# Performance work log

Hardware: AMD Instinct MI355X
Metric: run time of the kernel (lower is better)

Reference implementation:

```python
import jax, jax.numpy as jnp
import numpy as np

N_NODES = 50000
N_EDGES = 600000
IN_DIM = 128
HID = 128
OUT_DIM = 40
NUM_REL = 3
LN_EPS = 1e-5


def layer_norm(x, g, b):
    mu = jnp.mean(x, axis=-1, keepdims=True)
    var = jnp.var(x, axis=-1, keepdims=True)
    return (x - mu) * jax.lax.rsqrt(var + LN_EPS) * g + b


def rgcn_conv(x, edge_index, edge_type, w_rel, w_root, bias, aggr):
    """PyG-style RGCNConv: out = x @ W_root + bias + sum_r aggr_r(x_src @ W_r)."""
    src, dst = edge_index[0], edge_index[1]
    out = x @ w_root + bias                      # [N, F_out]
    for r in range(NUM_REL):                     # small fixed relation loop
        h = x @ w_rel[r]                         # transform-then-gather: [N, F_out]
        msg = h[src]                             # [E, F_out]
        mask = (edge_type == r)[:, None]
        if aggr == 'add':
            msg = jnp.where(mask, msg, 0.0)
            agg = jax.ops.segment_sum(msg, dst, num_segments=N_NODES)
        else:  # 'max'; empty segments -> 0 (matches PyG scatter_reduce include_self=False over zeros)
            msg = jnp.where(mask, msg, -jnp.inf)
            agg = jax.ops.segment_max(msg, dst, num_segments=N_NODES)
            agg = jnp.where(jnp.isfinite(agg), agg, 0.0)
        out = out + agg
    return out


def setup_inputs() -> dict:
    key = jax.random.key(0)
    ks = jax.random.split(key, 16)
    f32 = jnp.float32
    def lin(k, fan_in, shape):
        return jax.random.normal(k, shape, dtype=f32) / np.sqrt(fan_in)
    inp = {
        'x': jax.random.normal(ks[0], (N_NODES, IN_DIM), dtype=f32),
        'edge_index': jax.random.randint(ks[1], (2, N_EDGES), 0, N_NODES),
        'edge_type': jax.random.randint(ks[2], (N_EDGES,), 0, NUM_REL),
        # conv1
        'w1_rel': lin(ks[3], IN_DIM, (NUM_REL, IN_DIM, HID)),
        'w1_root': lin(ks[4], IN_DIM, (IN_DIM, HID)),
        'b1': jnp.zeros((HID,), f32),
        'ln1_g': jnp.ones((HID,), f32), 'ln1_b': jnp.zeros((HID,), f32),
        # conv2
        'w2_rel': lin(ks[5], HID, (NUM_REL, HID, HID)),
        'w2_root': lin(ks[6], HID, (HID, HID)),
        'b2': jnp.zeros((HID,), f32),
        'ln2_g': jnp.ones((HID,), f32), 'ln2_b': jnp.zeros((HID,), f32),
        # classifier
        'cw1': lin(ks[7], HID, (HID, HID)), 'cb1': jnp.zeros((HID,), f32),
        'cln1_g': jnp.ones((HID,), f32), 'cln1_b': jnp.zeros((HID,), f32),
        'cw2': lin(ks[8], HID, (HID, HID // 2)), 'cb2': jnp.zeros((HID // 2,), f32),
        'cln2_g': jnp.ones((HID // 2,), f32), 'cln2_b': jnp.zeros((HID // 2,), f32),
        'cw3': lin(ks[9], HID // 2, (HID // 2, OUT_DIM)), 'cb3': jnp.zeros((OUT_DIM,), f32),
    }
    return inp


def reference(x, edge_index, edge_type,
              w1_rel, w1_root, b1, ln1_g, ln1_b,
              w2_rel, w2_root, b2, ln2_g, ln2_b,
              cw1, cb1, cln1_g, cln1_b,
              cw2, cb2, cln2_g, cln2_b,
              cw3, cb3):
    # eval mode: edge dropout and feature dropout are identity
    h = rgcn_conv(x, edge_index, edge_type, w1_rel, w1_root, b1, 'add')
    h = jax.nn.relu(layer_norm(h, ln1_g, ln1_b))
    x1 = h
    h = rgcn_conv(x1, edge_index, edge_type, w2_rel, w2_root, b2, 'max')
    h = jax.nn.relu(layer_norm(h, ln2_g, ln2_b))
    h = h + x1 * 0.2
    # classifier MLP
    h = jax.nn.gelu(layer_norm(h @ cw1 + cb1, cln1_g, cln1_b), approximate=False)
    h = jax.nn.gelu(layer_norm(h @ cw2 + cb2, cln2_g, cln2_b), approximate=False)
    h = h @ cw3 + cb3
    return jax.nn.log_softmax(h, axis=1)
```

## Files before the change

kernel.cpp:

```cpp
#include <hip/hip_runtime.h>
#include <hip/hip_bf16.h>
#include <math.h>


typedef __attribute__((ext_vector_type(8))) short bf16x8;
typedef __attribute__((ext_vector_type(4))) float f32x4;
typedef unsigned short ushort_t;

__device__ __forceinline__ ushort_t bf16rne(float v) {
    unsigned u = __float_as_uint(v);
    return (ushort_t)((u + 0x7FFFu + ((u >> 16) & 1u)) >> 16);
}

__device__ __forceinline__ void split_bf16(float v, ushort_t& h, ushort_t& l) {
    ushort_t hu = bf16rne(v);
    float hf = __uint_as_float((unsigned)hu << 16);
    h = hu;
    l = bf16rne(v - hf);
}

__device__ __forceinline__ float bf2f(unsigned u16) {
    return __uint_as_float(u16 << 16);
}

__device__ __forceinline__ float4 unpack_bf4(uint2 u) {
    return make_float4(bf2f(u.x & 0xFFFFu), bf2f(u.x >> 16),
                       bf2f(u.y & 0xFFFFu), bf2f(u.y >> 16));
}

__device__ __forceinline__ uint2 pack_bf4(float4 v) {
    uint2 o;
    o.x = (unsigned)bf16rne(v.x) | ((unsigned)bf16rne(v.y) << 16);
    o.y = (unsigned)bf16rne(v.z) | ((unsigned)bf16rne(v.w) << 16);
    return o;
}

__device__ __forceinline__ void conv_body128(const float* __restrict__ W,
                                             ushort_t* __restrict__ out,
                                             int idx) {
    constexpr int NCF = 8;
    constexpr size_t PST = (size_t)4 * NCF * 512;
    int l = idx & 63;
    int cf = (idx >> 6) & 7;
    int ks = idx >> 9;
    int col = cf * 16 + (l & 15);
    int k0 = ks * 32 + (l >> 4) * 8;
    size_t base = (((size_t)ks * NCF + cf) * 64 + l) * 8;
#pragma unroll
    for (int j = 0; j < 8; ++j) {
        ushort_t h, lo_;
        split_bf16(W[(size_t)(k0 + j) * 128 + col], h, lo_);
        out[base + j] = h;
        out[PST + base + j] = lo_;
    }
}

__global__ __launch_bounds__(256) void convert_all(
    const float* __restrict__ w1_root, const float* __restrict__ w1_rel,
    const float* __restrict__ w2_root, const float* __restrict__ w2_rel,
    const float* __restrict__ cw1, const float* __restrict__ cw2,
    ushort_t* __restrict__ wfb) {
    int b = blockIdx.x;
    if (b < 72) {
        const float* src;
        int slot;
        if (b < 8)       { slot = 0;              src = w1_root; }
        else if (b < 32) { int r = (b - 8) >> 3;  slot = 1 + r; src = w1_rel + (size_t)r * 16384; }
        else if (b < 40) { slot = 4;              src = w2_root; }
        else if (b < 64) { int r = (b - 40) >> 3; slot = 5 + r; src = w2_rel + (size_t)r * 16384; }
        else             { slot = 8;              src = cw1; }
        int lb = (b < 8) ? b : (b < 32) ? ((b - 8) & 7) : (b < 40) ? (b - 32)
               : (b < 64) ? ((b - 40) & 7) : (b - 64);
        conv_body128(src, wfb + (size_t)slot * 32768, lb * 256 + threadIdx.x);
    } else {
        constexpr int NCF = 4;
        constexpr size_t PST = (size_t)4 * NCF * 512;
        int idx = (b - 72) * 256 + threadIdx.x;
        ushort_t* out = wfb + (size_t)9 * 32768;
        int l = idx & 63;
        int cf = (idx >> 6) & 3;
        int ks = idx >> 8;
        int col = cf * 16 + (l & 15);
        int k0 = ks * 32 + (l >> 4) * 8;
        size_t base = (((size_t)ks * NCF + cf) * 64 + l) * 8;
#pragma unroll
        for (int j = 0; j < 8; ++j) {
            ushort_t h, lo_;
            split_bf16(cw2[(size_t)(k0 + j) * 64 + col], h, lo_);
            out[base + j] = h;
            out[PST + base + j] = lo_;
        }
    }
}

__global__ __launch_bounds__(256) void x2bf(const float* __restrict__ x,
                                            ushort_t* __restrict__ xh, int n4) {
    int g = blockIdx.x * 256 + threadIdx.x;
    if (g >= n4) return;
    float4 v = ((const float4*)x)[g];
    ((uint2*)xh)[g] = pack_bf4(v);
}

template <int NCOL, int NSEG, int FUSE>
__global__ __launch_bounds__(256, 3) void gemm_bf(
    const ushort_t* __restrict__ A0, const ushort_t* __restrict__ A1,
    const ushort_t* __restrict__ A2, const ushort_t* __restrict__ A3,
    const ushort_t* __restrict__ wfrag, const float* __restrict__ bias,
    const float* __restrict__ lng, const float* __restrict__ lnb,
    void* __restrict__ Yv, int M) {
    constexpr int NCF = NCOL / 16;
    constexpr int WF = NCOL / 32;
    constexpr int PST = 4 * NCF * 512;
    constexpr int WSEG = 2 * PST;
    constexpr int RS = NCOL * 4 + 16;
    constexpr int EPB = 64 * RS;
    constexpr int SMEM_BYTES = (EPB > 16384) ? EPB : 16384;
    __shared__ __align__(16) char smem[SMEM_BYTES];
    char (*lds)[8192] = (char(*)[8192])smem;

    const int tid = threadIdx.x;
    const int wv = tid >> 6, lane = tid & 63, l15 = lane & 15, lg = lane >> 4;
    const int rowgrp = wv >> 1, colgrp = wv & 1;
    const int row0 = blockIdx.x * 64;
    const ushort_t* As[4] = {A0, A1, A2, A3};

    f32x4 acc[2][WF];
#pragma unroll
    for (int xf = 0; xf < 2; ++xf)
#pragma unroll
        for (int wf = 0; wf < WF; ++wf) acc[xf][wf] = (f32x4){0.f, 0.f, 0.f, 0.f};

    uint4 regs[2];

    auto LOADSTAGE = [&](int ch) {
        const ushort_t* __restrict__ A = As[ch >> 1];
        int kcb = (ch & 1) * 128;
#pragma unroll
        for (int i = 0; i < 2; ++i) {
            int s = tid + i * 256;
            int r = s >> 3, c16 = s & 7;
            int gr = row0 + r;
            uint4 v = make_uint4(0u, 0u, 0u, 0u);
            if (gr < M)
                v = *(const uint4*)((const char*)A + (size_t)gr * 256 + kcb + c16 * 16);
            regs[i] = v;
        }
    };

    auto WRITESTAGE = [&](int buf) {
        char* L = lds[buf];
#pragma unroll
        for (int i = 0; i < 2; ++i) {
            int s = tid + i * 256;
            int r = s >> 3, c16 = s & 7;
            int byte = (r * 128 + c16 * 16) ^ ((r & 7) << 4);
            *(uint4*)(L + byte) = regs[i];
        }
    };

    auto COMPUTE = [&](int ch, int buf) {
        int seg = ch >> 1, half = ch & 1;
        const ushort_t* __restrict__ ws = wfrag + (size_t)seg * WSEG;
        const char* L = lds[buf];
#pragma unroll
        for (int kk = 0; kk < 2; ++kk) {
            int ks = half * 2 + kk;
            bf16x8 xh[2];
#pragma unroll
            for (int xf = 0; xf < 2; ++xf) {
                int r = rowgrp * 32 + xf * 16 + l15;
                int byte = (r * 128 + kk * 64 + lg * 16) ^ ((r & 7) << 4);
                xh[xf] = *(const bf16x8*)(L + byte);
            }
            bf16x8 wh[WF], wl[WF];
#pragma unroll
            for (int wf = 0; wf < WF; ++wf) {
                size_t off = (((size_t)ks * NCF + colgrp * WF + wf) * 64 + lane) * 8;
                wh[wf] = *(const bf16x8*)(ws + off);
                wl[wf] = *(const bf16x8*)(ws + PST + off);
            }
#pragma unroll
            for (int xf = 0; xf < 2; ++xf)
#pragma unroll
                for (int wf = 0; wf < WF; ++wf) {
                    acc[xf][wf] = __builtin_amdgcn_mfma_f32_16x16x32_bf16(
                        wh[wf], xh[xf], acc[xf][wf], 0, 0, 0);
                    acc[xf][wf] = __builtin_amdgcn_mfma_f32_16x16x32_bf16(
                        wl[wf], xh[xf], acc[xf][wf], 0, 0, 0);
                }
        }
    };

    constexpr int CH = 2 * NSEG;
    LOADSTAGE(0);
    WRITESTAGE(0);
    __syncthreads();
    for (int ch = 0; ch < CH; ++ch) {
        if (ch + 1 < CH) LOADSTAGE(ch + 1);
        COMPUTE(ch, ch & 1);
        __syncthreads();
        if (ch + 1 < CH) WRITESTAGE((ch + 1) & 1);
        __syncthreads();
    }

    {
        float4 bv[WF];
#pragma unroll
        for (int wf = 0; wf < WF; ++wf) {
            int col = colgrp * (NCOL / 2) + wf * 16 + lg * 4;
            bv[wf] = bias ? *(const float4*)(bias + col)
                          : make_float4(0.f, 0.f, 0.f, 0.f);
        }
#pragma unroll
        for (int xf = 0; xf < 2; ++xf) {
            int r = rowgrp * 32 + xf * 16 + l15;
#pragma unroll
            for (int wf = 0; wf < WF; ++wf) {
                int col = colgrp * (NCOL / 2) + wf * 16 + lg * 4;
                float4 o;
                o.x = acc[xf][wf][0] + bv[wf].x;
                o.y = acc[xf][wf][1] + bv[wf].y;
                o.z = acc[xf][wf][2] + bv[wf].z;
                o.w = acc[xf][wf][3] + bv[wf].w;
                *(float4*)(smem + r * RS + col * 4) = o;
            }
        }
    }
    __syncthreads();

    if (FUSE >= 1 && FUSE <= 3) {
        constexpr int CPT = NCOL / 4;
        int r = tid >> 2, seg = tid & 3;
        char* rp = smem + r * RS + seg * CPT * 4;
        float s = 0.f, sq = 0.f;
        float4 vv[CPT / 4];
#pragma unroll
        for (int j = 0; j < CPT / 4; ++j) {
            float4 v = *(const float4*)(rp + j * 16);
            vv[j] = v;
            s += (v.x + v.y) + (v.z + v.w);
            sq += (v.x * v.x + v.y * v.y) + (v.z * v.z + v.w * v.w);
        }
        s += __shfl_xor(s, 1, 64); sq += __shfl_xor(sq, 1, 64);
        s += __shfl_xor(s, 2, 64); sq += __shfl_xor(sq, 2, 64);
        float mu = s * (1.f / NCOL);
        float var = sq * (1.f / NCOL) - mu * mu;
        float rstd = rsqrtf(var + 1e-5f);
#pragma unroll
        for (int j = 0; j < CPT / 4; ++j) {
            int c0 = seg * CPT + j * 4;
            float4 v = vv[j];
            float4 gg = *(const float4*)(lng + c0);
            float4 bb = *(const float4*)(lnb + c0);
            float y0 = (v.x - mu) * rstd * gg.x + bb.x;
            float y1 = (v.y - mu) * rstd * gg.y + bb.y;
            float y2 = (v.z - mu) * rstd * gg.z + bb.z;
            float y3 = (v.w - mu) * rstd * gg.w + bb.w;
            if (FUSE == 1) {
                y0 = fmaxf(y0, 0.f); y1 = fmaxf(y1, 0.f);
                y2 = fmaxf(y2, 0.f); y3 = fmaxf(y3, 0.f);
            } else {
                y0 = 0.5f * y0 * (1.f + erff(y0 * 0.70710678118654752f));
                y1 = 0.5f * y1 * (1.f + erff(y1 * 0.70710678118654752f));
                y2 = 0.5f * y2 * (1.f + erff(y2 * 0.70710678118654752f));
                y3 = 0.5f * y3 * (1.f + erff(y3 * 0.70710678118654752f));
            }
            vv[j] = make_float4(y0, y1, y2, y3);
        }
        __syncthreads();
        if (FUSE == 3) {
#pragma unroll
            for (int j = 0; j < CPT / 4; ++j) *(float4*)(rp + j * 16) = vv[j];
        } else {
#pragma unroll
            for (int j = 0; j < CPT / 4; ++j) {
                int c0 = seg * CPT + j * 4;
                *(uint2*)(smem + r * RS + 2 * c0) = pack_bf4(vv[j]);
            }
        }
        __syncthreads();
    }

    if (FUSE == 4) {
        constexpr int SL = 64 * (NCOL / 8);
#pragma unroll
        for (int i = 0; i < SL / 256; ++i) {
            int slot = tid + i * 256;
            int rr = slot / (NCOL / 8), c16 = slot % (NCOL / 8);
            int gr = row0 + rr;
            if (gr < M) {
                float4 a = *(const float4*)(smem + rr * RS + c16 * 32);
                float4 b = *(const float4*)(smem + rr * RS + c16 * 32 + 16);
                uint4 o;
                uint2 pa = pack_bf4(a), pb = pack_bf4(b);
                o.x = pa.x; o.y = pa.y; o.z = pb.x; o.w = pb.y;
                *(uint4*)((char*)Yv + (size_t)gr * (NCOL * 2) + c16 * 16) = o;
            }
        }
    } else {
        constexpr int OUTB = (FUSE == 0 || FUSE == 3) ? NCOL * 4 : NCOL * 2;
        constexpr int RP = OUTB / 16;
        constexpr int SL = 64 * RP;
#pragma unroll
        for (int i = 0; i < SL / 256; ++i) {
            int slot = tid + i * 256;
            int rr = slot / RP, c16 = slot % RP;
            int gr = row0 + rr;
            if (gr < M)
                *(uint4*)((char*)Yv + (size_t)gr * OUTB + c16 * 16) =
                    *(const uint4*)(smem + rr * RS + c16 * 16);
        }
    }
}

__global__ __launch_bounds__(256, 2) void gemm_conv2(
    const ushort_t* __restrict__ X, const ushort_t* __restrict__ wfb,
    const float* __restrict__ b2, ushort_t* __restrict__ ACbf,
    ushort_t* __restrict__ H0, ushort_t* __restrict__ H1,
    ushort_t* __restrict__ H2, int M) {
    constexpr int NCF = 8, WF = 4;
    constexpr int PST = 4 * NCF * 512;
    constexpr int RS2 = 256 + 16;
    __shared__ __align__(16) char smem[2 * 64 * RS2];
    char* Xs = smem;

    const int tid = threadIdx.x;
    const int wv = tid >> 6, lane = tid & 63, l15 = lane & 15, lg = lane >> 4;
    const int rowgrp = wv >> 1, colgrp = wv & 1;
    const int row0 = blockIdx.x * 64;

#pragma unroll
    for (int i = 0; i < 4; ++i) {
        int s = tid + i * 256;
        int r = s >> 4, c16 = s & 15;
        int gr = row0 + r;
        uint4 v = make_uint4(0u, 0u, 0u, 0u);
        if (gr < M) v = *(const uint4*)((const char*)X + (size_t)gr * 256 + c16 * 16);
        int byte = (r * 256 + c16 * 16) ^ ((r & 7) << 4);
        *(uint4*)(Xs + byte) = v;
    }
    __syncthreads();

    f32x4 acc[4][2][WF];
#pragma unroll
    for (int set = 0; set < 4; ++set)
#pragma unroll
        for (int xf = 0; xf < 2; ++xf)
#pragma unroll
            for (int wf = 0; wf < WF; ++wf)
                acc[set][xf][wf] = (f32x4){0.f, 0.f, 0.f, 0.f};

#pragma unroll
    for (int ks = 0; ks < 4; ++ks) {
        bf16x8 xh[2];
#pragma unroll
        for (int xf = 0; xf < 2; ++xf) {
            int r = rowgrp * 32 + xf * 16 + l15;
            int byte = (r * 256 + ks * 64 + lg * 16) ^ ((r & 7) << 4);
            xh[xf] = *(const bf16x8*)(Xs + byte);
        }
#pragma unroll
        for (int set = 0; set < 4; ++set) {
            const ushort_t* __restrict__ ws = wfb + (size_t)(4 + set) * 32768;
            bf16x8 wh[WF], wl[WF];
#pragma unroll
            for (int wf = 0; wf < WF; ++wf) {
                size_t off = (((size_t)ks * NCF + colgrp * WF + wf) * 64 + lane) * 8;
                wh[wf] = *(const bf16x8*)(ws + off);
                wl[wf] = *(const bf16x8*)(ws + PST + off);
            }
#pragma unroll
            for (int xf = 0; xf < 2; ++xf)
#pragma unroll
                for (int wf = 0; wf < WF; ++wf) {
                    acc[set][xf][wf] = __builtin_amdgcn_mfma_f32_16x16x32_bf16(
                        wh[wf], xh[xf], acc[set][xf][wf], 0, 0, 0);
                    acc[set][xf][wf] = __builtin_amdgcn_mfma_f32_16x16x32_bf16(
                        wl[wf], xh[xf], acc[set][xf][wf], 0, 0, 0);
                }
        }
    }
    __syncthreads();

    ushort_t* outs[4] = {ACbf, H0, H1, H2};
#pragma unroll
    for (int round = 0; round < 2; ++round) {
#pragma unroll
        for (int s2 = 0; s2 < 2; ++s2) {
            int set = round * 2 + s2;
            char* tile = smem + s2 * (64 * RS2);
#pragma unroll
            for (int xf = 0; xf < 2; ++xf) {
                int r = rowgrp * 32 + xf * 16 + l15;
#pragma unroll
                for (int wf = 0; wf < WF; ++wf) {
                    int col = colgrp * 64 + wf * 16 + lg * 4;
                    float4 o;
                    o.x = acc[set][xf][wf][0];
                    o.y = acc[set][xf][wf][1];
                    o.z = acc[set][xf][wf][2];
                    o.w = acc[set][xf][wf][3];
                    if (set == 0) {
                        float4 bv = *(const float4*)(b2 + col);
                        o.x += bv.x; o.y += bv.y; o.z += bv.z; o.w += bv.w;
                    }
                    *(uint2*)(tile + r * RS2 + col * 2) = pack_bf4(o);
                }
            }
        }
        __syncthreads();
#pragma unroll
        for (int s2 = 0; s2 < 2; ++s2) {
            int set = round * 2 + s2;
            ushort_t* O = outs[set];
            const char* tile = smem + s2 * (64 * RS2);
#pragma unroll
            for (int i = 0; i < 4; ++i) {
                int slot = tid + i * 256;
                int rr = slot >> 4, c16 = slot & 15;
                int gr = row0 + rr;
                if (gr < M)
                    *(uint4*)((char*)O + (size_t)gr * 256 + c16 * 16) =
                        *(const uint4*)(tile + rr * RS2 + c16 * 16);
            }
        }
        if (round == 0) __syncthreads();
    }
}

__global__ __launch_bounds__(256) void hist3_kernel(const int* __restrict__ edst,
                                                    const int* __restrict__ etype,
                                                    int* __restrict__ deg3, int E) {
    int e = blockIdx.x * 256 + threadIdx.x;
    if (e < E) atomicAdd(&deg3[edst[e] * 3 + etype[e]], 1);
}

__global__ __launch_bounds__(256) void degtot_kernel(const int* __restrict__ deg3,
                                                     int* __restrict__ degtot, int N) {
    int n = blockIdx.x * 256 + threadIdx.x;
    if (n < N) degtot[n] = deg3[n * 3] + deg3[n * 3 + 1] + deg3[n * 3 + 2];
}

__global__ __launch_bounds__(256) void scan_block(const int* __restrict__ in,
                                                  int* __restrict__ out,
                                                  int* __restrict__ sums, int n) {
    __shared__ int s[256];
    int g = blockIdx.x * 256 + threadIdx.x;
    int v = (g < n) ? in[g] : 0;
    s[threadIdx.x] = v;
    __syncthreads();
    int acc = v;
    for (int off = 1; off < 256; off <<= 1) {
        int t = (threadIdx.x >= off) ? s[threadIdx.x - off] : 0;
        __syncthreads();
        acc += t;
        s[threadIdx.x] = acc;
        __syncthreads();
    }
    if (g < n) out[g] = acc - v;
    if (threadIdx.x == 255 && sums) sums[blockIdx.x] = acc;
}

__global__ __launch_bounds__(256) void scan_add(int* __restrict__ out,
                                                const int* __restrict__ topex,
                                                int n, int total) {
    int g = blockIdx.x * 256 + threadIdx.x;
    if (g < n) out[g] += topex[blockIdx.x];
    if (g == 0) out[n] = total;
}

__global__ __launch_bounds__(256) void ranges_kernel(
    const int* __restrict__ rowptr, const int* __restrict__ deg3,
    int4* __restrict__ ranges, int* __restrict__ cursor3, int N) {
    int n = blockIdx.x * 256 + threadIdx.x;
    if (n >= N) return;
    int b = rowptr[n];
    int d0 = deg3[n * 3], d1 = deg3[n * 3 + 1];
    int4 r;
    r.x = b; r.y = b + d0; r.z = b + d0 + d1; r.w = rowptr[n + 1];
    ranges[n] = r;
    cursor3[n * 3] = r.x; cursor3[n * 3 + 1] = r.y; cursor3[n * 3 + 2] = r.z;
}

__global__ __launch_bounds__(256) void fill3_kernel(
    const int* __restrict__ esrc, const int* __restrict__ edst,
    const int* __restrict__ etype, int* __restrict__ cursor3,
    int* __restrict__ colidx, int E) {
    int e = blockIdx.x * 256 + threadIdx.x;
    if (e >= E) return;
    int pos = atomicAdd(&cursor3[edst[e] * 3 + etype[e]], 1);
    colidx[pos] = esrc[e];
}

__device__ __forceinline__ float4 gather_sum_bf(const ushort_t* __restrict__ XH,
                                                const int* __restrict__ colidx,
                                                int beg, int end, int l) {
    float4 a = make_float4(0.f, 0.f, 0.f, 0.f);
    int e = beg;
    for (; e + 4 <= end; e += 4) {
        int s0 = colidx[e], s1 = colidx[e + 1];
        int s2 = colidx[e + 2], s3 = colidx[e + 3];
        float4 v0 = unpack_bf4(*(const uint2*)(XH + (size_t)s0 * 128 + l * 4));
        float4 v1 = unpack_bf4(*(const uint2*)(XH + (size_t)s1 * 128 + l * 4));
        float4 v2 = unpack_bf4(*(const uint2*)(XH + (size_t)s2 * 128 + l * 4));
        float4 v3 = unpack_bf4(*(const uint2*)(XH + (size_t)s3 * 128 + l * 4));
        a.x += (v0.x + v1.x) + (v2.x + v3.x);
        a.y += (v0.y + v1.y) + (v2.y + v3.y);
        a.z += (v0.z + v1.z) + (v2.z + v3.z);
        a.w += (v0.w + v1.w) + (v2.w + v3.w);
    }
    for (; e < end; ++e) {
        float4 v = unpack_bf4(*(const uint2*)(XH + (size_t)colidx[e] * 128 + l * 4));
        a.x += v.x; a.y += v.y; a.z += v.z; a.w += v.w;
    }
    return a;
}

__global__ __launch_bounds__(256) void agg3_add(
    const ushort_t* __restrict__ xh, const int4* __restrict__ ranges,
    const int* __restrict__ colidx, ushort_t* __restrict__ S0,
    ushort_t* __restrict__ S1, ushort_t* __restrict__ S2, int N) {
    int node = blockIdx.x * 8 + (threadIdx.x >> 5);
    int l = threadIdx.x & 31;
    if (node >= N) return;
    int4 rg = ranges[node];
    float4 a0 = gather_sum_bf(xh, colidx, rg.x, rg.y, l);
    float4 a1 = gather_sum_bf(xh, colidx, rg.y, rg.z, l);
    float4 a2 = gather_sum_bf(xh, colidx, rg.z, rg.w, l);
    *(uint2*)(S0 + (size_t)node * 128 + l * 4) = pack_bf4(a0);
    *(uint2*)(S1 + (size_t)node * 128 + l * 4) = pack_bf4(a1);
    *(uint2*)(S2 + (size_t)node * 128 + l * 4) = pack_bf4(a2);
}

__device__ __forceinline__ float4 gather_max_bf(const ushort_t* __restrict__ H,
                                                const int* __restrict__ colidx,
                                                int beg, int end, int l) {
    float4 m = make_float4(-INFINITY, -INFINITY, -INFINITY, -INFINITY);
    int e = beg;
    for (; e + 4 <= end; e += 4) {
        int s0 = colidx[e], s1 = colidx[e + 1];
        int s2 = colidx[e + 2], s3 = colidx[e + 3];
        float4 v0 = unpack_bf4(*(const uint2*)(H + (size_t)s0 * 128 + l * 4));
        float4 v1 = unpack_bf4(*(const uint2*)(H + (size_t)s1 * 128 + l * 4));
        float4 v2 = unpack_bf4(*(const uint2*)(H + (size_t)s2 * 128 + l * 4));
        float4 v3 = unpack_bf4(*(const uint2*)(H + (size_t)s3 * 128 + l * 4));
        m.x = fmaxf(m.x, fmaxf(fmaxf(v0.x, v1.x), fmaxf(v2.x, v3.x)));
        m.y = fmaxf(m.y, fmaxf(fmaxf(v0.y, v1.y), fmaxf(v2.y, v3.y)));
        m.z = fmaxf(m.z, fmaxf(fmaxf(v0.z, v1.z), fmaxf(v2.z, v3.z)));
        m.w = fmaxf(m.w, fmaxf(fmaxf(v0.w, v1.w), fmaxf(v2.w, v3.w)));
    }
    for (; e < end; ++e) {
        float4 v = unpack_bf4(*(const uint2*)(H + (size_t)colidx[e] * 128 + l * 4));
        m.x = fmaxf(m.x, v.x); m.y = fmaxf(m.y, v.y);
        m.z = fmaxf(m.z, v.z); m.w = fmaxf(m.w, v.w);
    }
    m.x = (m.x > -3e38f) ? m.x : 0.f;
    m.y = (m.y > -3e38f) ? m.y : 0.f;
    m.z = (m.z > -3e38f) ? m.z : 0.f;
    m.w = (m.w > -3e38f) ? m.w : 0.f;
    return m;
}

__global__ __launch_bounds__(256) void maxagg_ln(
    const ushort_t* __restrict__ H0, const ushort_t* __restrict__ H1,
    const ushort_t* __restrict__ H2, const int4* __restrict__ ranges,
    const int* __restrict__ colidx, const ushort_t* __restrict__ accbf,
    const ushort_t* __restrict__ resid, const float* __restrict__ g,
    const float* __restrict__ b, ushort_t* __restrict__ outH, int N) {
    int node = blockIdx.x * 8 + (threadIdx.x >> 5);
    int l = threadIdx.x & 31;
    if (node >= N) return;
    int4 rg = ranges[node];
    float4 m0 = gather_max_bf(H0, colidx, rg.x, rg.y, l);
    float4 m1 = gather_max_bf(H1, colidx, rg.y, rg.z, l);
    float4 m2 = gather_max_bf(H2, colidx, rg.z, rg.w, l);
    float4 a = unpack_bf4(*(const uint2*)(accbf + (size_t)node * 128 + l * 4));
    a.x += m0.x + m1.x + m2.x;
    a.y += m0.y + m1.y + m2.y;
    a.z += m0.z + m1.z + m2.z;
    a.w += m0.w + m1.w + m2.w;
    float s = (a.x + a.y) + (a.z + a.w);
    float sq = (a.x * a.x + a.y * a.y) + (a.z * a.z + a.w * a.w);
#pragma unroll
    for (int off = 16; off; off >>= 1) {
        s += __shfl_xor(s, off, 64);
        sq += __shfl_xor(sq, off, 64);
    }
    float mu = s * (1.f / 128.f);
    float var = sq * (1.f / 128.f) - mu * mu;
    float rstd = rsqrtf(var + 1e-5f);
    float4 gg = *(const float4*)(g + l * 4);
    float4 bb = *(const float4*)(b + l * 4);
    float4 rv = unpack_bf4(*(const uint2*)(resid + (size_t)node * 128 + l * 4));
    float4 y;
    y.x = fmaxf((a.x - mu) * rstd * gg.x + bb.x, 0.f) + 0.2f * rv.x;
    y.y = fmaxf((a.y - mu) * rstd * gg.y + bb.y, 0.f) + 0.2f * rv.y;
    y.z = fmaxf((a.z - mu) * rstd * gg.z + bb.z, 0.f) + 0.2f * rv.z;
    y.w = fmaxf((a.w - mu) * rstd * gg.w + bb.w, 0.f) + 0.2f * rv.w;
    *(uint2*)(outH + (size_t)node * 128 + l * 4) = pack_bf4(y);
}

__global__ __launch_bounds__(256) void gemm40_lsm(const float* __restrict__ X,
                                                  const float* __restrict__ W,
                                                  const float* __restrict__ bias,
                                                  float* __restrict__ Y, int M) {
    __shared__ float Xs[64][65];
    __shared__ float Ws[64 * 40];
    __shared__ float Ys[64][41];
    __shared__ float mx_[64], ls_[64];
    const int tid = threadIdx.x;
    const int row0 = blockIdx.x * 64;
    for (int i = tid; i < 64 * 40; i += 256) Ws[i] = W[i];
#pragma unroll
    for (int i = 0; i < 4; ++i) {
        int slot = tid + i * 256;
        int r = slot >> 4, c4 = slot & 15;
        float4 v = make_float4(0.f, 0.f, 0.f, 0.f);
        if (row0 + r < M) v = *(const float4*)(X + (size_t)(row0 + r) * 64 + c4 * 4);
        Xs[r][c4 * 4 + 0] = v.x; Xs[r][c4 * 4 + 1] = v.y;
        Xs[r][c4 * 4 + 2] = v.z; Xs[r][c4 * 4 + 3] = v.w;
    }
    __syncthreads();
    const int row = tid >> 2, cg = (tid & 3) * 10;
    float acc[10];
#pragma unroll
    for (int j = 0; j < 10; ++j) acc[j] = 0.f;
#pragma unroll 8
    for (int k = 0; k < 64; ++k) {
        float xv = Xs[row][k];
#pragma unroll
        for (int j = 0; j < 10; ++j) acc[j] = fmaf(xv, Ws[k * 40 + cg + j], acc[j]);
    }
#pragma unroll
    for (int j = 0; j < 10; ++j) Ys[row][cg + j] = acc[j] + bias[cg + j];
    __syncthreads();
    if (tid < 64) {
        float mx = -INFINITY;
#pragma unroll 8
        for (int c = 0; c < 40; ++c) mx = fmaxf(mx, Ys[tid][c]);
        float sum = 0.f;
#pragma unroll 8
        for (int c = 0; c < 40; ++c) sum += __expf(Ys[tid][c] - mx);
        mx_[tid] = mx;
        ls_[tid] = logf(sum);
    }
    __syncthreads();
#pragma unroll
    for (int i = 0; i < 10; ++i) {
        int slot = tid + i * 256;
        int r = slot / 40, c = slot % 40;
        int gr = row0 + r;
        if (gr < M) Y[(size_t)gr * 40 + c] = Ys[r][c] - mx_[r] - ls_[r];
    }
}

extern "C" void kernel_launch(void* const* d_in, const int* in_sizes, int n_in,
                              void* d_out, int out_size, void* d_ws, size_t ws_size,
                              hipStream_t stream) {
    const float* x       = (const float*)d_in[0];
    const int*   eidx    = (const int*)d_in[1];
    const int*   etype   = (const int*)d_in[2];
    const float* w1_rel  = (const float*)d_in[3];
    const float* w1_root = (const float*)d_in[4];
    const float* b1      = (const float*)d_in[5];
    const float* ln1_g   = (const float*)d_in[6];
    const float* ln1_b   = (const float*)d_in[7];
    const float* w2_rel  = (const float*)d_in[8];
    const float* w2_root = (const float*)d_in[9];
    const float* b2      = (const float*)d_in[10];
    const float* ln2_g   = (const float*)d_in[11];
    const float* ln2_b   = (const float*)d_in[12];
    const float* cw1     = (const float*)d_in[13];
    const float* cb1     = (const float*)d_in[14];
    const float* cln1_g  = (const float*)d_in[15];
    const float* cln1_b  = (const float*)d_in[16];
    const float* cw2     = (const float*)d_in[17];
    const float* cb2     = (const float*)d_in[18];
    const float* cln2_g  = (const float*)d_in[19];
    const float* cln2_b  = (const float*)d_in[20];
    const float* cw3     = (const float*)d_in[21];
    const float* cb3     = (const float*)d_in[22];

    const int N = in_sizes[0] / 128;
    const int E = in_sizes[1] / 2;
    const int* esrc = eidx;
    const int* edst = eidx + E;

    const size_t HB = (size_t)N * 256;
    char* base = (char*)d_ws;
    ushort_t* S0 = (ushort_t*)(base + 0 * HB);
    ushort_t* S1 = (ushort_t*)(base + 1 * HB);
    ushort_t* S2 = (ushort_t*)(base + 2 * HB);
    ushort_t* X1 = (ushort_t*)(base + 3 * HB);
    ushort_t* AC = (ushort_t*)(base + 4 * HB);
    char*     B3 = base + 5 * HB;

    int* rowptr  = (int*)B3;
    int* degtot  = rowptr + (N + 1);
    int* deg3    = degtot + N;
    int* cursor3 = deg3 + 3 * N;
    int* bsums   = cursor3 + 3 * N;
    int* btop    = bsums + 256;
    int4* ranges = (int4*)(((uintptr_t)(btop + 256) + 15) & ~(uintptr_t)15);
    int* colidx  = (int*)(ranges + N);
    ushort_t* wfb = (ushort_t*)(((uintptr_t)(colidx + E) + 255) & ~(uintptr_t)255);
    auto WSLOT = [&](int i) { return wfb + (size_t)i * 32768; };
    ushort_t* xh = (ushort_t*)(((uintptr_t)(wfb + 10 * 32768) + 255) & ~(uintptr_t)255);
    ushort_t* h2 = xh;
    ushort_t* C1 = S0;
    float*    C2 = (float*)S1;

    const dim3 blk(256);
    const int gGemm = (N + 63) / 64;
    const int gAgg  = (N + 7) / 8;
    const int gEdge = (E + 255) / 256;
    const int gNode = (N + 255) / 256;
    const int nScanB = (N + 255) / 256;
    const int gX2  = (N * 32 + 255) / 256;

    hipMemsetAsync(deg3, 0, (size_t)3 * N * sizeof(int), stream);
    hist3_kernel<<<gEdge, blk, 0, stream>>>(edst, etype, deg3, E);
    degtot_kernel<<<gNode, blk, 0, stream>>>(deg3, degtot, N);
    scan_block<<<nScanB, blk, 0, stream>>>(degtot, rowptr, bsums, N);
    scan_block<<<1, blk, 0, stream>>>(bsums, btop, nullptr, nScanB);
    scan_add<<<nScanB, blk, 0, stream>>>(rowptr, btop, N, E);
    ranges_kernel<<<gNode, blk, 0, stream>>>(rowptr, deg3, ranges, cursor3, N);
    fill3_kernel<<<gEdge, blk, 0, stream>>>(esrc, edst, etype, cursor3, colidx, E);

    convert_all<<<76, blk, 0, stream>>>(w1_root, w1_rel, w2_root, w2_rel,
                                        cw1, cw2, wfb);
    x2bf<<<gX2, blk, 0, stream>>>(x, xh, N * 32);

    agg3_add<<<gAgg, blk, 0, stream>>>(xh, ranges, colidx, S0, S1, S2, N);
    gemm_bf<128, 4, 1><<<gGemm, blk, 0, stream>>>(
        xh, S0, S1, S2, WSLOT(0), b1, ln1_g, ln1_b, X1, N);

    gemm_conv2<<<gGemm, blk, 0, stream>>>(X1, wfb, b2, AC, S0, S1, S2, N);
    maxagg_ln<<<gAgg, blk, 0, stream>>>(S0, S1, S2, ranges, colidx, AC,
                                        X1, ln2_g, ln2_b, h2, N);

    gemm_bf<128, 1, 2><<<gGemm, blk, 0, stream>>>(
        h2, h2, h2, h2, WSLOT(8), cb1, cln1_g, cln1_b, C1, N);
    gemm_bf<64, 1, 3><<<gGemm, blk, 0, stream>>>(
        C1, C1, C1, C1, WSLOT(9), cb2, cln2_g, cln2_b, C2, N);
    gemm40_lsm<<<gGemm, blk, 0, stream>>>(C2, cw3, cb3, (float*)d_out, N);
}
```

Before: 289.8 us.

## Process conv2 weight sets sequentially to cut accumulators and raise occupancy

The conv2 GEMM now computes and writes out one of the four output sets at a time instead of holding all four sets of accumulators at once. It reuses a single epilogue staging tile in shared memory, separate from the X tile, and raises the launch-bounds occupancy hint from 2 to 3 blocks per SM. The goal is lower register and LDS pressure so more waves can hide memory latency. In exchange, the X fragments are reloaded from LDS for every set, there are more barriers, and the four weight streams no longer overlap within one k-step.

Measured after the change: 266.9 us. 1.09x faster.

```diff
diff --git a/kernel.cpp b/kernel.cpp
--- a/kernel.cpp
+++ b/kernel.cpp
@@ -313,7 +313,7 @@
     }
 }
 
-__global__ __launch_bounds__(256, 2) void gemm_conv2(
+__global__ __launch_bounds__(256, 3) void gemm_conv2(
     const ushort_t* __restrict__ X, const ushort_t* __restrict__ wfb,
     const float* __restrict__ b2, ushort_t* __restrict__ ACbf,
     ushort_t* __restrict__ H0, ushort_t* __restrict__ H1,
@@ -321,8 +321,9 @@
     constexpr int NCF = 8, WF = 4;
     constexpr int PST = 4 * NCF * 512;
     constexpr int RS2 = 256 + 16;
-    __shared__ __align__(16) char smem[2 * 64 * RS2];
+    __shared__ __align__(16) char smem[16384 + 64 * RS2];
     char* Xs = smem;
+    char* ep = smem + 16384;
 
     const int tid = threadIdx.x;
     const int wv = tid >> 6, lane = tid & 63, l15 = lane & 15, lg = lane >> 4;
@@ -341,27 +342,23 @@
     }
     __syncthreads();
 
-    f32x4 acc[4][2][WF];
-#pragma unroll
-    for (int set = 0; set < 4; ++set)
+    ushort_t* outs[4] = {ACbf, H0, H1, H2};
+    for (int set = 0; set < 4; ++set) {
+        const ushort_t* __restrict__ ws = wfb + (size_t)(4 + set) * 32768;
+        f32x4 acc[2][WF];
 #pragma unroll
         for (int xf = 0; xf < 2; ++xf)
 #pragma unroll
-            for (int wf = 0; wf < WF; ++wf)
-                acc[set][xf][wf] = (f32x4){0.f, 0.f, 0.f, 0.f};
-
-#pragma unroll
-    for (int ks = 0; ks < 4; ++ks) {
-        bf16x8 xh[2];
-#pragma unroll
-        for (int xf = 0; xf < 2; ++xf) {
-            int r = rowgrp * 32 + xf * 16 + l15;
-            int byte = (r * 256 + ks * 64 + lg * 16) ^ ((r & 7) << 4);
-            xh[xf] = *(const bf16x8*)(Xs + byte);
-        }
-#pragma unroll
-        for (int set = 0; set < 4; ++set) {
-            const ushort_t* __restrict__ ws = wfb + (size_t)(4 + set) * 32768;
+            for (int wf = 0; wf < WF; ++wf) acc[xf][wf] = (f32x4){0.f, 0.f, 0.f, 0.f};
+#pragma unroll
+        for (int ks = 0; ks < 4; ++ks) {
+            bf16x8 xh[2];
+#pragma unroll
+            for (int xf = 0; xf < 2; ++xf) {
+                int r = rowgrp * 32 + xf * 16 + l15;
+                int byte = (r * 256 + ks * 64 + lg * 16) ^ ((r & 7) << 4);
+                xh[xf] = *(const bf16x8*)(Xs + byte);
+            }
             bf16x8 wh[WF], wl[WF];
 #pragma unroll
             for (int wf = 0; wf < WF; ++wf) {
@@ -373,58 +370,42 @@
             for (int xf = 0; xf < 2; ++xf)
 #pragma unroll
                 for (int wf = 0; wf < WF; ++wf) {
-                    acc[set][xf][wf] = __builtin_amdgcn_mfma_f32_16x16x32_bf16(
-                        wh[wf], xh[xf], acc[set][xf][wf], 0, 0, 0);
-                    acc[set][xf][wf] = __builtin_amdgcn_mfma_f32_16x16x32_bf16(
-                        wl[wf], xh[xf], acc[set][xf][wf], 0, 0, 0);
+                    acc[xf][wf] = __builtin_amdgcn_mfma_f32_16x16x32_bf16(
+                        wh[wf], xh[xf], acc[xf][wf], 0, 0, 0);
+                    acc[xf][wf] = __builtin_amdgcn_mfma_f32_16x16x32_bf16(
+                        wl[wf], xh[xf], acc[xf][wf], 0, 0, 0);
                 }
         }
-    }
-    __syncthreads();
-
-    ushort_t* outs[4] = {ACbf, H0, H1, H2};
-#pragma unroll
-    for (int round = 0; round < 2; ++round) {
-#pragma unroll
-        for (int s2 = 0; s2 < 2; ++s2) {
-            int set = round * 2 + s2;
-            char* tile = smem + s2 * (64 * RS2);
-#pragma unroll
-            for (int xf = 0; xf < 2; ++xf) {
-                int r = rowgrp * 32 + xf * 16 + l15;
-#pragma unroll
-                for (int wf = 0; wf < WF; ++wf) {
-                    int col = colgrp * 64 + wf * 16 + lg * 4;
-                    float4 o;
-                    o.x = acc[set][xf][wf][0];
-                    o.y = acc[set][xf][wf][1];
-                    o.z = acc[set][xf][wf][2];
-                    o.w = acc[set][xf][wf][3];
-                    if (set == 0) {
-                        float4 bv = *(const float4*)(b2 + col);
-                        o.x += bv.x; o.y += bv.y; o.z += bv.z; o.w += bv.w;
-                    }
-                    *(uint2*)(tile + r * RS2 + col * 2) = pack_bf4(o);
+        __syncthreads();
+#pragma unroll
+        for (int xf = 0; xf < 2; ++xf) {
+            int r = rowgrp * 32 + xf * 16 + l15;
+#pragma unroll
+            for (int wf = 0; wf < WF; ++wf) {
+                int col = colgrp * 64 + wf * 16 + lg * 4;
+                float4 o;
+                o.x = acc[xf][wf][0];
+                o.y = acc[xf][wf][1];
+                o.z = acc[xf][wf][2];
+                o.w = acc[xf][wf][3];
+                if (set == 0) {
+                    float4 bv = *(const float4*)(b2 + col);
+                    o.x += bv.x; o.y += bv.y; o.z += bv.z; o.w += bv.w;
                 }
+                *(uint2*)(ep + r * RS2 + col * 2) = pack_bf4(o);
             }
         }
         __syncthreads();
-#pragma unroll
-        for (int s2 = 0; s2 < 2; ++s2) {
-            int set = round * 2 + s2;
-            ushort_t* O = outs[set];
-            const char* tile = smem + s2 * (64 * RS2);
-#pragma unroll
-            for (int i = 0; i < 4; ++i) {
-                int slot = tid + i * 256;
-                int rr = slot >> 4, c16 = slot & 15;
-                int gr = row0 + rr;
-                if (gr < M)
-                    *(uint4*)((char*)O + (size_t)gr * 256 + c16 * 16) =
-                        *(const uint4*)(tile + rr * RS2 + c16 * 16);
-            }
-        }
-        if (round == 0) __syncthreads();
+        ushort_t* O = outs[set];
+#pragma unroll
+        for (int i = 0; i < 4; ++i) {
+            int slot = tid + i * 256;
+            int rr = slot >> 4, c16 = slot & 15;
+            int gr = row0 + rr;
+            if (gr < M)
+                *(uint4*)((char*)O + (size_t)gr * 256 + c16 * 16) =
+                    *(const uint4*)(ep + rr * RS2 + c16 * 16);
+        }
     }
 }
 
```
